# Kernel tuning notes

Measured on AMD Instinct MI355X. Metric: run time of the kernel, lower is better.

Reference implementation:

```python
import jax, jax.numpy as jnp
import numpy as np

LN_EPS = 1e-5
EPSILON = 1e-8
NUM_ITERS = 3
SLOT_SIZE = 128
NUM_SLOTS = 7
MLP_HIDDEN = 256


def _layernorm(x, g, b):
    m = jnp.mean(x, axis=-1, keepdims=True)
    v = jnp.var(x, axis=-1, keepdims=True)
    return (x - m) * jax.lax.rsqrt(v + LN_EPS) * g + b


def setup_inputs() -> dict:
    key = jax.random.key(0)
    ks = jax.random.split(key, 16)
    B, N, D, S, H, M = 64, 4096, 128, NUM_SLOTS, SLOT_SIZE, MLP_HIDDEN
    sc = 0.05
    return {
        "inputs": jax.random.normal(ks[0], (B, N, D), jnp.float32),
        "slots_init": jax.random.normal(ks[1], (B, S, H + 4), jnp.float32),
        "ln_in_g": jnp.ones((D,), jnp.float32), "ln_in_b": jnp.zeros((D,), jnp.float32),
        "ln_s_g": jnp.ones((H,), jnp.float32), "ln_s_b": jnp.zeros((H,), jnp.float32),
        "ln_m_g": jnp.ones((H,), jnp.float32), "ln_m_b": jnp.zeros((H,), jnp.float32),
        "Wq": jax.random.normal(ks[2], (H, H), jnp.float32) * sc,
        "Wk": jax.random.normal(ks[3], (H, H), jnp.float32) * sc,
        "Wv": jax.random.normal(ks[4], (H, H), jnp.float32) * sc,
        "W_ih": jax.random.normal(ks[5], (3 * H, H), jnp.float32) * sc,
        "W_hh": jax.random.normal(ks[6], (3 * H, H), jnp.float32) * sc,
        "b_ih": jnp.zeros((3 * H,), jnp.float32),
        "b_hh": jnp.zeros((3 * H,), jnp.float32),
        "mlp_w1": jax.random.normal(ks[7], (M, H), jnp.float32) * sc,
        "mlp_b1": jnp.zeros((M,), jnp.float32),
        "mlp_w2": jax.random.normal(ks[8], (H, M), jnp.float32) * sc,
        "mlp_b2": jnp.zeros((H,), jnp.float32),
        "slots_mu": jax.random.normal(ks[9], (1, 1, H + 4), jnp.float32) * sc,
        "slots_log_sigma": jax.random.normal(ks[10], (1, 1, H + 4), jnp.float32) * sc,
    }


def _gru_cell(x, h, W_ih, W_hh, b_ih, b_hh):
    # torch.nn.GRUCell math; x, h: [..., H]
    gi = x @ W_ih.T + b_ih
    gh = h @ W_hh.T + b_hh
    i_r, i_z, i_n = jnp.split(gi, 3, axis=-1)
    h_r, h_z, h_n = jnp.split(gh, 3, axis=-1)
    r = jax.nn.sigmoid(i_r + h_r)
    z = jax.nn.sigmoid(i_z + h_z)
    n = jnp.tanh(i_n + r * h_n)
    return (1.0 - z) * n + z * h


def reference(inputs, slots_init, ln_in_g, ln_in_b, ln_s_g, ln_s_b, ln_m_g, ln_m_b,
              Wq, Wk, Wv, W_ih, W_hh, b_ih, b_hh, mlp_w1, mlp_b1, mlp_w2, mlp_b2,
              slots_mu, slots_log_sigma):
    x = _layernorm(inputs, ln_in_g, ln_in_b)           # [B, N, D]
    k = x @ Wk.T                                       # [B, N, H]
    v = x @ Wv.T                                       # [B, N, H]
    slots_full = slots_mu + jnp.exp(slots_log_sigma) * slots_init  # [B, S, H+4]
    slots = slots_full[..., :SLOT_SIZE]                # positions/scales discarded
    scale = SLOT_SIZE ** -0.5
    for _ in range(NUM_ITERS):
        slots_prev = slots
        sn = _layernorm(slots, ln_s_g, ln_s_b)
        q = sn @ Wq.T                                  # [B, S, H]
        logits = scale * jnp.einsum('bnh,bsh->bns', k, q)
        attn = jax.nn.softmax(logits, axis=-1) + EPSILON
        attn = attn / jnp.sum(attn, axis=1, keepdims=True)
        updates = jnp.einsum('bns,bnh->bsh', attn, v)  # [B, S, H]
        slots = _gru_cell(updates, slots_prev, W_ih, W_hh, b_ih, b_hh)
        slots = slots + (jax.nn.relu(_layernorm(slots, ln_m_g, ln_m_b) @ mlp_w1.T + mlp_b1) @ mlp_w2.T + mlp_b2)
    return slots
```

## Files before the change

### kernel.cpp

```cpp
#include <hip/hip_runtime.h>
#include <hip/hip_bf16.h>
#include <stdint.h>

typedef unsigned int u32;
typedef unsigned short u16;
typedef float v2f __attribute__((ext_vector_type(2)));
typedef short bf16x8 __attribute__((ext_vector_type(8)));
typedef float f32x4 __attribute__((ext_vector_type(4)));

#define LN_EPS_ 1e-5f
#define EPS_ 1e-8f

__device__ __forceinline__ float bflo(u32 v){ return __uint_as_float(v << 16); }
__device__ __forceinline__ float bfhi(u32 v){ return __uint_as_float(v & 0xFFFF0000u); }
__device__ __forceinline__ u32 f2bf(float f){
    u32 x = __float_as_uint(f);
    return (x + 0x7FFFu + ((x >> 16) & 1u)) >> 16;
}
__device__ __forceinline__ u32 pack2bf(float a, float b){
    union { __hip_bfloat162 h; u32 u; } cv;
    cv.h = __float22bfloat162_rn(float2{a, b});
    return cv.u;
}
__device__ __forceinline__ v2f pkfma(v2f a, v2f b, v2f c){
    v2f d; asm("v_pk_fma_f32 %0, %1, %2, %3" : "=v"(d) : "v"(a), "v"(b), "v"(c)); return d;
}
__device__ __forceinline__ v2f pkadd(v2f a, v2f b){
    v2f d; asm("v_pk_add_f32 %0, %1, %2" : "=v"(d) : "v"(a), "v"(b)); return d;
}
__device__ __forceinline__ bf16x8 as_bf16x8(uint4 u){
    union { uint4 a; bf16x8 b; } c; c.a = u; return c.b;
}

__global__ __launch_bounds__(256) void k_pack(
    const float* __restrict__ Wq, const float* __restrict__ Wv,
    const float* __restrict__ Wih, const float* __restrict__ Whh,
    const float* __restrict__ w1, const float* __restrict__ w2,
    float* __restrict__ WqT, u32* __restrict__ Pv, u32* __restrict__ Pih,
    u32* __restrict__ Phh, u32* __restrict__ Pw1, u32* __restrict__ Pw2,
    u32* __restrict__ Rg32)
{
    int i = blockIdx.x * 256 + threadIdx.x;
    if (i < 8192) {
        int dp = i >> 7, o = i & 127;
        Pv[i] = pack2bf(Wv[o * 128 + 2 * dp], Wv[o * 128 + 2 * dp + 1]);
    } else if (i < 32768) {
        int r = i - 8192; int dp = r / 384, j = r - dp * 384;
        Pih[r] = pack2bf(Wih[j * 128 + 2 * dp], Wih[j * 128 + 2 * dp + 1]);
    } else if (i < 57344) {
        int r = i - 32768; int dp = r / 384, j = r - dp * 384;
        Phh[r] = pack2bf(Whh[j * 128 + 2 * dp], Whh[j * 128 + 2 * dp + 1]);
    } else if (i < 73728) {
        int r = i - 57344; int dp = r >> 8, j = r & 255;
        Pw1[r] = pack2bf(w1[j * 128 + 2 * dp], w1[j * 128 + 2 * dp + 1]);
    } else if (i < 90112) {
        int r = i - 73728; int mp = r >> 7, o = r & 127;
        Pw2[r] = pack2bf(w2[o * 256 + 2 * mp], w2[o * 256 + 2 * mp + 1]);
    } else if (i < 106496) {
        int r = i - 90112; int d = r >> 7, o = r & 127;
        WqT[r] = Wq[o * 128 + d];
    } else if (i < 143360) {
        int r = i - 106496; int b = r / 576, rem = r - b * 576;
        Rg32[b * 1024 + 448 + rem] = 0;
    }
}

__device__ __forceinline__ void prep_tail(
    int b, int s, int h, int half, int t, float nv,
    const float* __restrict__ g_s, const float* __restrict__ b_s,
    const float* __restrict__ WqT, const float* __restrict__ Wk,
    const float* __restrict__ g_in, const float* __restrict__ b_in,
    u16* __restrict__ Rg, float* __restrict__ c1ws, float* __restrict__ c2ws,
    float* snb, float* qb, float* xch, float* red4)
{
    if (!half) {
        float smv = nv, sqv = nv * nv;
        for (int m = 32; m >= 1; m >>= 1) { smv += __shfl_xor(smv, m); sqv += __shfl_xor(sqv, m); }
        if ((t & 63) == 0) { red4[(t >> 6) * 2] = smv; red4[(t >> 6) * 2 + 1] = sqv; }
    }
    __syncthreads();
    float mean = (red4[0] + red4[2]) * (1.0f / 128.0f);
    float var  = (red4[1] + red4[3]) * (1.0f / 128.0f) - mean * mean;
    float rsv = rsqrtf(var + LN_EPS_);
    if (!half) snb[h] = (nv - mean) * rsv * g_s[h] + b_s[h];
    __syncthreads();
    {
        float q0 = 0.f, q1 = 0.f;
        int d0 = half * 64;
        #pragma unroll 4
        for (int d = d0; d < d0 + 64; d += 2) {
            q0 += WqT[d * 128 + h] * snb[d];
            q1 += WqT[(d + 1) * 128 + h] * snb[d + 1];
        }
        if (half) xch[h] = q0 + q1;
        __syncthreads();
        if (!half) qb[h] = q0 + q1 + xch[h];
        __syncthreads();
    }
    float r0 = 0.f, r1 = 0.f;
    int j0 = half * 64;
    #pragma unroll 4
    for (int j = j0; j < j0 + 64; j += 2) {
        r0 += Wk[j * 128 + h] * qb[j];
        r1 += Wk[(j + 1) * 128 + h] * qb[j + 1];
    }
    if (half) xch[h] = r0 + r1;
    __syncthreads();
    if (!half) {
        float r = (r0 + r1 + xch[h]) * 0.08838834764831845f;
        float rt  = g_in[h] * r;
        float c2v = b_in[h] * r;
        Rg[((size_t)b * 16 + s) * 128 + h] = (u16)f2bf(rt);
        float c1p = rt, c2p = c2v;
        for (int m = 32; m >= 1; m >>= 1) { c1p += __shfl_xor(c1p, m); c2p += __shfl_xor(c2p, m); }
        if ((t & 63) == 0) { red4[(t >> 6) * 2] = c1p; red4[(t >> 6) * 2 + 1] = c2p; }
    }
    __syncthreads();
    if (t == 0) {
        c1ws[b * 8 + s] = red4[0] + red4[2];
        c2ws[b * 8 + s] = red4[1] + red4[3];
    }
}

__global__ __launch_bounds__(256) void k_init_prep(
    const float* __restrict__ slots_init, const float* __restrict__ mu,
    const float* __restrict__ ls, float* __restrict__ slots,
    const float* __restrict__ g_s, const float* __restrict__ b_s,
    const float* __restrict__ WqT, const float* __restrict__ Wk,
    const float* __restrict__ g_in, const float* __restrict__ b_in,
    u16* __restrict__ Rg, float* __restrict__ c1ws, float* __restrict__ c2ws)
{
    __shared__ float snb[128], qb[128], xch[128], red4[4];
    int bs = blockIdx.x, t = threadIdx.x;
    int b = bs / 7, s = bs - b * 7;
    int h = t & 127, half = t >> 7;
    float nv = 0.f;
    if (!half) {
        nv = mu[h] + expf(ls[h]) * slots_init[bs * 132 + h];
        slots[bs * 128 + h] = nv;
    }
    prep_tail(b, s, h, half, t, nv, g_s, b_s, WqT, Wk, g_in, b_in,
              Rg, c1ws, c2ws, snb, qb, xch, red4);
}

__global__ __launch_bounds__(256, 8) void k_attn(
    const float* __restrict__ xin,
    const u16* __restrict__ Rg, const float* __restrict__ c1ws,
    const float* __restrict__ c2ws,
    float* __restrict__ ypart, float* __restrict__ Zp, float* __restrict__ Ap)
{
    __shared__ u32 tile[4096];
    __shared__ __align__(16) float wt[448];
    __shared__ __align__(8)  float stats[128];
    __shared__ float c1l[16], c2l[16];
    __shared__ float redp[4][8], redw[4][8];
    int t = threadIdx.x;
    int b = blockIdx.y;
    int n0 = blockIdx.x * 64;
    int lane = t & 63, wv = t >> 6;
    int ls = lane & 15, lg = lane >> 4;

    if (t < 16) {
        c1l[t] = (t < 7) ? c1ws[b * 8 + t] : 0.f;
        c2l[t] = (t < 7) ? c2ws[b * 8 + t] : 0.f;
    }

    bf16x8 bfr[4];
    {
        const u16* Rrow = Rg + ((size_t)b * 16 + ls) * 128;
        #pragma unroll
        for (int kk = 0; kk < 4; kk++)
            bfr[kk] = as_bf16x8(*(const uint4*)&Rrow[kk * 32 + lg * 8]);
    }

    {
        int r = t >> 2, p = t & 3;
        const float4* xg = (const float4*)(xin + ((size_t)b * 4096 + n0 + r) * 128 + p * 32);
        v2f smp = (v2f){0.f, 0.f}, sqp = (v2f){0.f, 0.f};
        #pragma unroll
        for (int i = 0; i < 8; i++) {
            float4 v = xg[i];
            v2f lo = (v2f){v.x, v.y}, hi = (v2f){v.z, v.w};
            smp = pkadd(smp, pkadd(lo, hi));
            sqp = pkfma(lo, lo, sqp);
            sqp = pkfma(hi, hi, sqp);
            int q = p * 4 + (i >> 1), rem = (i & 1) * 2;
            *(uint2*)&tile[(r * 16 + (q ^ (r & 15))) * 4 + rem] =
                make_uint2(pack2bf(v.x, v.y), pack2bf(v.z, v.w));
        }
        float sm = smp.x + smp.y, sq = sqp.x + sqp.y;
        sm += __shfl_xor(sm, 1); sq += __shfl_xor(sq, 1);
        sm += __shfl_xor(sm, 2); sq += __shfl_xor(sq, 2);
        if (!p) {
            float mean = sm * (1.0f / 128.0f);
            float var  = sq * (1.0f / 128.0f) - mean * mean;
            *(float2*)&stats[2 * r] = make_float2(mean, rsqrtf(var + LN_EPS_));
        }
    }
    __syncthreads();

    f32x4 acc0 = {0.f, 0.f, 0.f, 0.f};
    {
        int m0 = wv * 16 + ls;
        #pragma unroll
        for (int kk = 0; kk < 4; kk++) {
            int q = kk * 4 + lg;
            bf16x8 a0 = as_bf16x8(*(const uint4*)&tile[(m0 * 16 + (q ^ ls)) * 4]);
            acc0 = __builtin_amdgcn_mfma_f32_16x16x32_bf16(a0, bfr[kk], acc0, 0, 0, 0);
        }
    }
    {
        float zsum = 0.f, asum = 0.f;
        float c1v = c1l[ls], c2v = c2l[ls];
        bool sv = ls < 7;
        int nbase = wv * 16 + lg * 4;
        #pragma unroll
        for (int r4 = 0; r4 < 4; r4++) {
            int n = nbase + r4;
            float2 stf = *(const float2*)&stats[2 * n];
            float L = sv ? (stf.y * (acc0[r4] - stf.x * c1v) + c2v) : -3.4e38f;
            float mx = L;
            mx = fmaxf(mx, __shfl_xor(mx, 1));
            mx = fmaxf(mx, __shfl_xor(mx, 2));
            mx = fmaxf(mx, __shfl_xor(mx, 4));
            mx = fmaxf(mx, __shfl_xor(mx, 8));
            float e = __expf(L - mx);
            float ssum = e;
            ssum += __shfl_xor(ssum, 1);
            ssum += __shfl_xor(ssum, 2);
            ssum += __shfl_xor(ssum, 4);
            ssum += __shfl_xor(ssum, 8);
            float p = e * (1.0f / ssum) + EPS_;
            float w = p * stf.y;
            if (sv) {
                wt[ls * 64 + n] = w;
                zsum += p;
                asum += w * stf.x;
            }
        }
        zsum += __shfl_xor(zsum, 16); zsum += __shfl_xor(zsum, 32);
        asum += __shfl_xor(asum, 16); asum += __shfl_xor(asum, 32);
        if (lane < 7) { redp[wv][lane] = zsum; redw[wv][lane] = asum; }
    }
    __syncthreads();
    if (t < 7)
        Zp[((size_t)b * 64 + blockIdx.x) * 8 + t] =
            redp[0][t] + redp[1][t] + redp[2][t] + redp[3][t];
    else if (t >= 64 && t < 71) {
        int s = t - 64;
        Ap[((size_t)b * 64 + blockIdx.x) * 8 + s] =
            redw[0][s] + redw[1][s] + redw[2][s] + redw[3][s];
    }

    int nh = t >> 7, dp = t & 63, sA = (t >> 6) & 1;
    v2f aclo[4], achi[4];
    #pragma unroll
    for (int k = 0; k < 4; k++) { aclo[k] = (v2f){0.f,0.f}; achi[k] = (v2f){0.f,0.f}; }
    int nbeg = nh * 32;
    #pragma unroll 4
    for (int n = nbeg; n < nbeg + 32; n += 2) {
        u32 x0 = tile[(n * 16 + ((dp >> 2) ^ (n & 15))) * 4 + (dp & 3)];
        u32 x1 = tile[((n + 1) * 16 + ((dp >> 2) ^ ((n + 1) & 15))) * 4 + (dp & 3)];
        v2f alo = (v2f){bflo(x0), bflo(x1)};
        v2f ahi = (v2f){bfhi(x0), bfhi(x1)};
        #pragma unroll
        for (int k = 0; k < 4; k++) {
            int s = sA + 2 * k;
            if (s < 7) {
                v2f wp = *(const v2f*)&wt[s * 64 + n];
                aclo[k] = pkfma(alo, wp, aclo[k]);
                achi[k] = pkfma(ahi, wp, achi[k]);
            }
        }
    }
    float* yp = ypart + (((size_t)b * 64 + blockIdx.x) * 2 + nh) * 896;
    #pragma unroll
    for (int k = 0; k < 4; k++) {
        int s = sA + 2 * k;
        if (s < 7) {
            *(float2*)&yp[s * 128 + 2 * dp] =
                make_float2(aclo[k].x + aclo[k].y, achi[k].x + achi[k].y);
        }
    }
}

__global__ __launch_bounds__(256) void k_update(
    float* __restrict__ slots, const float* __restrict__ ypart,
    const float* __restrict__ Zp, const float* __restrict__ Ap,
    const float* __restrict__ g_in, const float* __restrict__ b_in,
    const u32* __restrict__ Pv, const u32* __restrict__ Pih,
    const u32* __restrict__ Phh, const float* __restrict__ b_ih,
    const float* __restrict__ b_hh, const float* __restrict__ g_m,
    const float* __restrict__ b_m, const u32* __restrict__ Pw1,
    const float* __restrict__ bb1, const u32* __restrict__ Pw2,
    const float* __restrict__ bb2, float* __restrict__ out,
    const float* __restrict__ g_s, const float* __restrict__ b_s,
    const float* __restrict__ WqT, const float* __restrict__ Wk,
    u16* __restrict__ Rg, float* __restrict__ c1ws, float* __restrict__ c2ws,
    int do_prep)
{
    __shared__ float ybuf[128], ub[128], hb[128], lb[128], t1b[256];
    __shared__ float ghx[384];
    __shared__ float up[128], op[128];
    __shared__ float redA[2], redB[2];
    __shared__ float snb[128], qb[128], xch[128], red4[4];
    __shared__ float Zsh, Ash;
    int bs = blockIdx.x, t = threadIdx.x;
    int b = bs / 7, s = bs - b * 7;
    int h = t & 127, half = t >> 7;
    float ysum = 0.f;
    {
        const float* bp = ypart + ((size_t)(b * 128 + half * 64)) * 896 + s * 128 + h;
        #pragma unroll 8
        for (int c = 0; c < 64; c++) ysum += bp[(size_t)c * 896];
    }
    if (t < 64) {
        float z = Zp[((size_t)b * 64 + t) * 8 + s];
        for (int m = 32; m >= 1; m >>= 1) z += __shfl_xor(z, m);
        if (t == 0) Zsh = z;
    } else if (t < 128) {
        float a_ = Ap[((size_t)b * 64 + (t - 64)) * 8 + s];
        for (int m = 32; m >= 1; m >>= 1) a_ += __shfl_xor(a_, m);
        if (t == 64) Ash = a_;
    }
    if (half) up[h] = ysum;
    __syncthreads();
    if (!half) {
        float ytot = ysum + up[h];
        ybuf[h] = g_in[h] * (ytot - Ash) / Zsh + b_in[h];
        hb[h] = slots[bs * 128 + h];
    }
    __syncthreads();
    {
        float a0 = 0.f, a1 = 0.f;
        int dp0 = half * 32;
        #pragma unroll 4
        for (int dp = dp0; dp < dp0 + 32; dp += 2) {
            u32 w0 = Pv[dp * 128 + h];
            u32 w1v = Pv[(dp + 1) * 128 + h];
            a0 += bflo(w0) * ybuf[2 * dp] + bfhi(w0) * ybuf[2 * dp + 1];
            a1 += bflo(w1v) * ybuf[2 * dp + 2] + bfhi(w1v) * ybuf[2 * dp + 3];
        }
        if (half) up[h] = a0 + a1;
        __syncthreads();
        if (!half) ub[h] = (a0 + a1) + up[h];
        __syncthreads();
    }
    float gv0, gv1, gv2;
    {
        const u32* P = half ? Phh : Pih;
        const float* src = half ? hb : ub;
        gv0 = half ? b_hh[h] : b_ih[h];
        gv1 = half ? b_hh[128 + h] : b_ih[128 + h];
        gv2 = half ? b_hh[256 + h] : b_ih[256 + h];
        #pragma unroll 4
        for (int dp = 0; dp < 64; dp++) {
            float x0 = src[2 * dp], x1 = src[2 * dp + 1];
            u32 w0 = P[dp * 384 + h];
            u32 w1v = P[dp * 384 + 128 + h];
            u32 w2v = P[dp * 384 + 256 + h];
            gv0 += bflo(w0) * x0 + bfhi(w0) * x1;
            gv1 += bflo(w1v) * x0 + bfhi(w1v) * x1;
            gv2 += bflo(w2v) * x0 + bfhi(w2v) * x1;
        }
        if (half) { ghx[h] = gv0; ghx[128 + h] = gv1; ghx[256 + h] = gv2; }
    }
    __syncthreads();
    float hv = 0.f;
    if (!half) {
        float rg = 1.0f / (1.0f + __expf(-(gv0 + ghx[h])));
        float zg = 1.0f / (1.0f + __expf(-(gv1 + ghx[128 + h])));
        float ng = tanhf(gv2 + rg * ghx[256 + h]);
        hv = (1.0f - zg) * ng + zg * hb[h];
        float sm2 = hv, sq2 = hv * hv;
        for (int m = 32; m >= 1; m >>= 1) { sm2 += __shfl_xor(sm2, m); sq2 += __shfl_xor(sq2, m); }
        if ((t & 63) == 0) { redA[t >> 6] = sm2; redB[t >> 6] = sq2; }
    }
    __syncthreads();
    if (!half) {
        float sm2 = redA[0] + redA[1], sq2 = redB[0] + redB[1];
        float mean = sm2 * (1.0f / 128.0f);
        float var  = sq2 * (1.0f / 128.0f) - mean * mean;
        float rsq = rsqrtf(var + LN_EPS_);
        lb[h] = (hv - mean) * rsq * g_m[h] + b_m[h];
    }
    __syncthreads();
    {
        float m1 = bb1[t];
        #pragma unroll 4
        for (int dp = 0; dp < 64; dp++) {
            u32 w0 = Pw1[dp * 256 + t];
            m1 += bflo(w0) * lb[2 * dp] + bfhi(w0) * lb[2 * dp + 1];
        }
        t1b[t] = fmaxf(m1, 0.0f);
    }
    __syncthreads();
    float nv = 0.f;
    {
        float o0 = 0.f, o1 = 0.f;
        int mp0 = half * 64;
        #pragma unroll 4
        for (int mp = mp0; mp < mp0 + 64; mp += 2) {
            u32 w0 = Pw2[mp * 128 + h];
            u32 w1v = Pw2[(mp + 1) * 128 + h];
            o0 += bflo(w0) * t1b[2 * mp] + bfhi(w0) * t1b[2 * mp + 1];
            o1 += bflo(w1v) * t1b[2 * mp + 2] + bfhi(w1v) * t1b[2 * mp + 3];
        }
        if (half) op[h] = o0 + o1;
        __syncthreads();
        if (!half) {
            nv = hv + bb2[h] + (o0 + o1) + op[h];
            slots[bs * 128 + h] = nv;
            out[bs * 128 + h] = nv;
        }
    }
    if (do_prep) {
        __syncthreads();
        prep_tail(b, s, h, half, t, nv, g_s, b_s, WqT, Wk, g_in, b_in,
                  Rg, c1ws, c2ws, snb, qb, xch, red4);
    }
}

extern "C" void kernel_launch(void* const* d_in, const int* in_sizes, int n_in,
                              void* d_out, int out_size, void* d_ws, size_t ws_size,
                              hipStream_t stream) {
    const float* inputs     = (const float*)d_in[0];
    const float* slots_init = (const float*)d_in[1];
    const float* ln_in_g    = (const float*)d_in[2];
    const float* ln_in_b    = (const float*)d_in[3];
    const float* ln_s_g     = (const float*)d_in[4];
    const float* ln_s_b     = (const float*)d_in[5];
    const float* ln_m_g     = (const float*)d_in[6];
    const float* ln_m_b     = (const float*)d_in[7];
    const float* Wq         = (const float*)d_in[8];
    const float* Wk         = (const float*)d_in[9];
    const float* Wv         = (const float*)d_in[10];
    const float* W_ih       = (const float*)d_in[11];
    const float* W_hh       = (const float*)d_in[12];
    const float* b_ih       = (const float*)d_in[13];
    const float* b_hh       = (const float*)d_in[14];
    const float* mlp_w1     = (const float*)d_in[15];
    const float* mlp_b1     = (const float*)d_in[16];
    const float* mlp_w2     = (const float*)d_in[17];
    const float* mlp_b2     = (const float*)d_in[18];
    const float* slots_mu   = (const float*)d_in[19];
    const float* slots_ls   = (const float*)d_in[20];

    char* ws = (char*)d_ws;
    float* slots = (float*)(ws);
    u16*   Rg    = (u16*)  (ws + 229376);
    float* c1ws  = (float*)(ws + 491520);
    float* c2ws  = (float*)(ws + 493568);
    float* WqT   = (float*)(ws + 495616);
    u32*   Pv    = (u32*)  (ws + 561152);
    u32*   Pih   = (u32*)  (ws + 593920);
    u32*   Phh   = (u32*)  (ws + 692224);
    u32*   Pw1   = (u32*)  (ws + 790528);
    u32*   Pw2   = (u32*)  (ws + 856064);
    float* Zp    = (float*)(ws + 921600);
    float* Ap    = (float*)(ws + 1052672);
    float* ypart = (float*)(ws + 1183744);

    k_pack<<<560, 256, 0, stream>>>(Wq, Wv, W_ih, W_hh, mlp_w1, mlp_w2,
                                    WqT, Pv, Pih, Phh, Pw1, Pw2, (u32*)Rg);
    k_init_prep<<<448, 256, 0, stream>>>(slots_init, slots_mu, slots_ls, slots,
                                         ln_s_g, ln_s_b, WqT, Wk, ln_in_g, ln_in_b,
                                         Rg, c1ws, c2ws);
    for (int it = 0; it < 3; it++) {
        k_attn<<<dim3(64, 64), 256, 0, stream>>>(inputs, Rg, c1ws, c2ws,
                                                 ypart, Zp, Ap);
        k_update<<<448, 256, 0, stream>>>(slots, ypart, Zp, Ap, ln_in_g, ln_in_b,
                                          Pv, Pih, Phh, b_ih, b_hh,
                                          ln_m_g, ln_m_b, Pw1, mlp_b1, Pw2, mlp_b2,
                                          (float*)d_out,
                                          ln_s_g, ln_s_b, WqT, Wk,
                                          Rg, c1ws, c2ws, (it < 2) ? 1 : 0);
    }
}
```

Before: 388.4 us.

## Cache bf16 swizzled input tiles and LN stats after first attention pass

On the first attention iteration, each block writes its already-swizzled bf16 tile and per-row layernorm stats to a workspace buffer. Later iterations reload these instead of re-reading the fp32 inputs and recomputing statistics, halving input bytes per pass. The update kernel also moves from 256 to 512 threads, splitting each matvec four ways with shared-memory reductions. The trade-off is extra workspace traffic on the first pass, and it assumes the workspace is large enough at the new offsets.

```diff
diff --git a/kernel.cpp b/kernel.cpp
--- a/kernel.cpp
+++ b/kernel.cpp
@@ -65,63 +65,6 @@
     }
 }
 
-__device__ __forceinline__ void prep_tail(
-    int b, int s, int h, int half, int t, float nv,
-    const float* __restrict__ g_s, const float* __restrict__ b_s,
-    const float* __restrict__ WqT, const float* __restrict__ Wk,
-    const float* __restrict__ g_in, const float* __restrict__ b_in,
-    u16* __restrict__ Rg, float* __restrict__ c1ws, float* __restrict__ c2ws,
-    float* snb, float* qb, float* xch, float* red4)
-{
-    if (!half) {
-        float smv = nv, sqv = nv * nv;
-        for (int m = 32; m >= 1; m >>= 1) { smv += __shfl_xor(smv, m); sqv += __shfl_xor(sqv, m); }
-        if ((t & 63) == 0) { red4[(t >> 6) * 2] = smv; red4[(t >> 6) * 2 + 1] = sqv; }
-    }
-    __syncthreads();
-    float mean = (red4[0] + red4[2]) * (1.0f / 128.0f);
-    float var  = (red4[1] + red4[3]) * (1.0f / 128.0f) - mean * mean;
-    float rsv = rsqrtf(var + LN_EPS_);
-    if (!half) snb[h] = (nv - mean) * rsv * g_s[h] + b_s[h];
-    __syncthreads();
-    {
-        float q0 = 0.f, q1 = 0.f;
-        int d0 = half * 64;
-        #pragma unroll 4
-        for (int d = d0; d < d0 + 64; d += 2) {
-            q0 += WqT[d * 128 + h] * snb[d];
-            q1 += WqT[(d + 1) * 128 + h] * snb[d + 1];
-        }
-        if (half) xch[h] = q0 + q1;
-        __syncthreads();
-        if (!half) qb[h] = q0 + q1 + xch[h];
-        __syncthreads();
-    }
-    float r0 = 0.f, r1 = 0.f;
-    int j0 = half * 64;
-    #pragma unroll 4
-    for (int j = j0; j < j0 + 64; j += 2) {
-        r0 += Wk[j * 128 + h] * qb[j];
-        r1 += Wk[(j + 1) * 128 + h] * qb[j + 1];
-    }
-    if (half) xch[h] = r0 + r1;
-    __syncthreads();
-    if (!half) {
-        float r = (r0 + r1 + xch[h]) * 0.08838834764831845f;
-        float rt  = g_in[h] * r;
-        float c2v = b_in[h] * r;
-        Rg[((size_t)b * 16 + s) * 128 + h] = (u16)f2bf(rt);
-        float c1p = rt, c2p = c2v;
-        for (int m = 32; m >= 1; m >>= 1) { c1p += __shfl_xor(c1p, m); c2p += __shfl_xor(c2p, m); }
-        if ((t & 63) == 0) { red4[(t >> 6) * 2] = c1p; red4[(t >> 6) * 2 + 1] = c2p; }
-    }
-    __syncthreads();
-    if (t == 0) {
-        c1ws[b * 8 + s] = red4[0] + red4[2];
-        c2ws[b * 8 + s] = red4[1] + red4[3];
-    }
-}
-
 __global__ __launch_bounds__(256) void k_init_prep(
     const float* __restrict__ slots_init, const float* __restrict__ mu,
     const float* __restrict__ ls, float* __restrict__ slots,
@@ -139,15 +82,61 @@
         nv = mu[h] + expf(ls[h]) * slots_init[bs * 132 + h];
         slots[bs * 128 + h] = nv;
     }
-    prep_tail(b, s, h, half, t, nv, g_s, b_s, WqT, Wk, g_in, b_in,
-              Rg, c1ws, c2ws, snb, qb, xch, red4);
+    if (!half) {
+        float smv = nv, sqv = nv * nv;
+        for (int m = 32; m >= 1; m >>= 1) { smv += __shfl_xor(smv, m); sqv += __shfl_xor(sqv, m); }
+        if ((t & 63) == 0) { red4[(t >> 6) * 2] = smv; red4[(t >> 6) * 2 + 1] = sqv; }
+    }
+    __syncthreads();
+    float mean = (red4[0] + red4[2]) * (1.0f / 128.0f);
+    float var  = (red4[1] + red4[3]) * (1.0f / 128.0f) - mean * mean;
+    float rsv = rsqrtf(var + LN_EPS_);
+    if (!half) snb[h] = (nv - mean) * rsv * g_s[h] + b_s[h];
+    __syncthreads();
+    {
+        float q0 = 0.f, q1 = 0.f;
+        int d0 = half * 64;
+        #pragma unroll 4
+        for (int d = d0; d < d0 + 64; d += 2) {
+            q0 += WqT[d * 128 + h] * snb[d];
+            q1 += WqT[(d + 1) * 128 + h] * snb[d + 1];
+        }
+        if (half) xch[h] = q0 + q1;
+        __syncthreads();
+        if (!half) qb[h] = q0 + q1 + xch[h];
+        __syncthreads();
+    }
+    float r0 = 0.f, r1 = 0.f;
+    int j0 = half * 64;
+    #pragma unroll 4
+    for (int j = j0; j < j0 + 64; j += 2) {
+        r0 += Wk[j * 128 + h] * qb[j];
+        r1 += Wk[(j + 1) * 128 + h] * qb[j + 1];
+    }
+    if (half) xch[h] = r0 + r1;
+    __syncthreads();
+    if (!half) {
+        float r = (r0 + r1 + xch[h]) * 0.08838834764831845f;
+        float rt  = g_in[h] * r;
+        float c2v = b_in[h] * r;
+        Rg[((size_t)b * 16 + s) * 128 + h] = (u16)f2bf(rt);
+        float c1p = rt, c2p = c2v;
+        for (int m = 32; m >= 1; m >>= 1) { c1p += __shfl_xor(c1p, m); c2p += __shfl_xor(c2p, m); }
+        if ((t & 63) == 0) { red4[(t >> 6) * 2] = c1p; red4[(t >> 6) * 2 + 1] = c2p; }
+    }
+    __syncthreads();
+    if (t == 0) {
+        c1ws[b * 8 + s] = red4[0] + red4[2];
+        c2ws[b * 8 + s] = red4[1] + red4[3];
+    }
 }
 
 __global__ __launch_bounds__(256, 8) void k_attn(
     const float* __restrict__ xin,
     const u16* __restrict__ Rg, const float* __restrict__ c1ws,
     const float* __restrict__ c2ws,
-    float* __restrict__ ypart, float* __restrict__ Zp, float* __restrict__ Ap)
+    float* __restrict__ ypart, float* __restrict__ Zp, float* __restrict__ Ap,
+    u32* __restrict__ Xbf, float* __restrict__ Sg, int first)
 {
     __shared__ u32 tile[4096];
     __shared__ __align__(16) float wt[448];
@@ -159,6 +148,7 @@
     int n0 = blockIdx.x * 64;
     int lane = t & 63, wv = t >> 6;
     int ls = lane & 15, lg = lane >> 4;
+    size_t blk = (size_t)b * 64 + blockIdx.x;
 
     if (t < 16) {
         c1l[t] = (t < 7) ? c1ws[b * 8 + t] : 0.f;
@@ -173,7 +163,7 @@
             bfr[kk] = as_bf16x8(*(const uint4*)&Rrow[kk * 32 + lg * 8]);
     }
 
-    {
+    if (first) {
         int r = t >> 2, p = t & 3;
         const float4* xg = (const float4*)(xin + ((size_t)b * 4096 + n0 + r) * 128 + p * 32);
         v2f smp = (v2f){0.f, 0.f}, sqp = (v2f){0.f, 0.f};
@@ -196,8 +186,20 @@
             float var  = sq * (1.0f / 128.0f) - mean * mean;
             *(float2*)&stats[2 * r] = make_float2(mean, rsqrtf(var + LN_EPS_));
         }
-    }
-    __syncthreads();
+        __syncthreads();
+        uint4* dst = (uint4*)(Xbf + blk * 4096);
+        const uint4* srcT = (const uint4*)tile;
+        #pragma unroll
+        for (int j = 0; j < 4; j++) dst[j * 256 + t] = srcT[j * 256 + t];
+        if (t < 128) Sg[blk * 128 + t] = stats[t];
+    } else {
+        uint4* dstT = (uint4*)tile;
+        const uint4* src = (const uint4*)(Xbf + blk * 4096);
+        #pragma unroll
+        for (int j = 0; j < 4; j++) dstT[j * 256 + t] = src[j * 256 + t];
+        if (t < 128) stats[t] = Sg[blk * 128 + t];
+        __syncthreads();
+    }
 
     f32x4 acc0 = {0.f, 0.f, 0.f, 0.f};
     {
@@ -244,12 +246,10 @@
     }
     __syncthreads();
     if (t < 7)
-        Zp[((size_t)b * 64 + blockIdx.x) * 8 + t] =
-            redp[0][t] + redp[1][t] + redp[2][t] + redp[3][t];
+        Zp[blk * 8 + t] = redp[0][t] + redp[1][t] + redp[2][t] + redp[3][t];
     else if (t >= 64 && t < 71) {
         int s = t - 64;
-        Ap[((size_t)b * 64 + blockIdx.x) * 8 + s] =
-            redw[0][s] + redw[1][s] + redw[2][s] + redw[3][s];
+        Ap[blk * 8 + s] = redw[0][s] + redw[1][s] + redw[2][s] + redw[3][s];
     }
 
     int nh = t >> 7, dp = t & 63, sA = (t >> 6) & 1;
@@ -273,7 +273,7 @@
             }
         }
     }
-    float* yp = ypart + (((size_t)b * 64 + blockIdx.x) * 2 + nh) * 896;
+    float* yp = ypart + (blk * 2 + nh) * 896;
     #pragma unroll
     for (int k = 0; k < 4; k++) {
         int s = sA + 2 * k;
@@ -284,7 +284,7 @@
     }
 }
 
-__global__ __launch_bounds__(256) void k_update(
+__global__ __launch_bounds__(512) void k_update(
     float* __restrict__ slots, const float* __restrict__ ypart,
     const float* __restrict__ Zp, const float* __restrict__ Ap,
     const float* __restrict__ g_in, const float* __restrict__ b_in,
@@ -300,19 +300,21 @@
     int do_prep)
 {
     __shared__ float ybuf[128], ub[128], hb[128], lb[128], t1b[256];
-    __shared__ float ghx[384];
-    __shared__ float up[128], op[128];
+    __shared__ float red4w[4][128];
+    __shared__ float g6[12][128];
+    __shared__ float m1p[256];
     __shared__ float redA[2], redB[2];
-    __shared__ float snb[128], qb[128], xch[128], red4[4];
+    __shared__ float snb[128], qb[128], red4[4];
     __shared__ float Zsh, Ash;
     int bs = blockIdx.x, t = threadIdx.x;
     int b = bs / 7, s = bs - b * 7;
-    int h = t & 127, half = t >> 7;
-    float ysum = 0.f;
-    {
-        const float* bp = ypart + ((size_t)(b * 128 + half * 64)) * 896 + s * 128 + h;
+    int h = t & 127, q = t >> 7;
+    {
+        float ysum = 0.f;
+        const float* bp = ypart + ((size_t)(b * 128 + q * 32)) * 896 + s * 128 + h;
         #pragma unroll 8
-        for (int c = 0; c < 64; c++) ysum += bp[(size_t)c * 896];
+        for (int c = 0; c < 32; c++) ysum += bp[(size_t)c * 896];
+        red4w[q][h] = ysum;
     }
     if (t < 64) {
         float z = Zp[((size_t)b * 64 + t) * 8 + s];
@@ -323,38 +325,33 @@
         for (int m = 32; m >= 1; m >>= 1) a_ += __shfl_xor(a_, m);
         if (t == 64) Ash = a_;
     }
-    if (half) up[h] = ysum;
-    __syncthreads();
-    if (!half) {
-        float ytot = ysum + up[h];
+    __syncthreads();
+    if (q == 0) {
+        float ytot = red4w[0][h] + red4w[1][h] + red4w[2][h] + red4w[3][h];
         ybuf[h] = g_in[h] * (ytot - Ash) / Zsh + b_in[h];
         hb[h] = slots[bs * 128 + h];
     }
     __syncthreads();
     {
-        float a0 = 0.f, a1 = 0.f;
-        int dp0 = half * 32;
+        float a0 = 0.f;
+        int dp0 = q * 16;
         #pragma unroll 4
-        for (int dp = dp0; dp < dp0 + 32; dp += 2) {
+        for (int dp = dp0; dp < dp0 + 16; dp++) {
             u32 w0 = Pv[dp * 128 + h];
-            u32 w1v = Pv[(dp + 1) * 128 + h];
             a0 += bflo(w0) * ybuf[2 * dp] + bfhi(w0) * ybuf[2 * dp + 1];
-            a1 += bflo(w1v) * ybuf[2 * dp + 2] + bfhi(w1v) * ybuf[2 * dp + 3];
-        }
-        if (half) up[h] = a0 + a1;
-        __syncthreads();
-        if (!half) ub[h] = (a0 + a1) + up[h];
-        __syncthreads();
-    }
-    float gv0, gv1, gv2;
-    {
-        const u32* P = half ? Phh : Pih;
-        const float* src = half ? hb : ub;
-        gv0 = half ? b_hh[h] : b_ih[h];
-        gv1 = half ? b_hh[128 + h] : b_ih[128 + h];
-        gv2 = half ? b_hh[256 + h] : b_ih[256 + h];
+        }
+        red4w[q][h] = a0;
+    }
+    __syncthreads();
+    if (q == 0) ub[h] = red4w[0][h] + red4w[1][h] + red4w[2][h] + red4w[3][h];
+    __syncthreads();
+    {
+        const u32* P = (q >= 2) ? Phh : Pih;
+        const float* src = (q >= 2) ? hb : ub;
+        int dp0 = (q & 1) * 32;
+        float gv0 = 0.f, gv1 = 0.f, gv2 = 0.f;
         #pragma unroll 4
-        for (int dp = 0; dp < 64; dp++) {
+        for (int dp = dp0; dp < dp0 + 32; dp++) {
             float x0 = src[2 * dp], x1 = src[2 * dp + 1];
             u32 w0 = P[dp * 384 + h];
             u32 w1v = P[dp * 384 + 128 + h];
@@ -363,21 +360,27 @@
             gv1 += bflo(w1v) * x0 + bfhi(w1v) * x1;
             gv2 += bflo(w2v) * x0 + bfhi(w2v) * x1;
         }
-        if (half) { ghx[h] = gv0; ghx[128 + h] = gv1; ghx[256 + h] = gv2; }
+        g6[q * 3 + 0][h] = gv0; g6[q * 3 + 1][h] = gv1; g6[q * 3 + 2][h] = gv2;
     }
     __syncthreads();
     float hv = 0.f;
-    if (!half) {
-        float rg = 1.0f / (1.0f + __expf(-(gv0 + ghx[h])));
-        float zg = 1.0f / (1.0f + __expf(-(gv1 + ghx[128 + h])));
-        float ng = tanhf(gv2 + rg * ghx[256 + h]);
+    if (q == 0) {
+        float gi0 = g6[0][h] + g6[3][h] + b_ih[h];
+        float gi1 = g6[1][h] + g6[4][h] + b_ih[128 + h];
+        float gi2 = g6[2][h] + g6[5][h] + b_ih[256 + h];
+        float gh0 = g6[6][h] + g6[9][h]  + b_hh[h];
+        float gh1 = g6[7][h] + g6[10][h] + b_hh[128 + h];
+        float gh2 = g6[8][h] + g6[11][h] + b_hh[256 + h];
+        float rg = 1.0f / (1.0f + __expf(-(gi0 + gh0)));
+        float zg = 1.0f / (1.0f + __expf(-(gi1 + gh1)));
+        float ng = tanhf(gi2 + rg * gh2);
         hv = (1.0f - zg) * ng + zg * hb[h];
         float sm2 = hv, sq2 = hv * hv;
         for (int m = 32; m >= 1; m >>= 1) { sm2 += __shfl_xor(sm2, m); sq2 += __shfl_xor(sq2, m); }
         if ((t & 63) == 0) { redA[t >> 6] = sm2; redB[t >> 6] = sq2; }
     }
     __syncthreads();
-    if (!half) {
+    if (q == 0) {
         float sm2 = redA[0] + redA[1], sq2 = redB[0] + redB[1];
         float mean = sm2 * (1.0f / 128.0f);
         float var  = sq2 * (1.0f / 128.0f) - mean * mean;
@@ -386,38 +389,82 @@
     }
     __syncthreads();
     {
-        float m1 = bb1[t];
+        int o = t & 255, kh = t >> 8;
+        float m1 = 0.f;
+        int dp0 = kh * 32;
         #pragma unroll 4
-        for (int dp = 0; dp < 64; dp++) {
-            u32 w0 = Pw1[dp * 256 + t];
+        for (int dp = dp0; dp < dp0 + 32; dp++) {
+            u32 w0 = Pw1[dp * 256 + o];
             m1 += bflo(w0) * lb[2 * dp] + bfhi(w0) * lb[2 * dp + 1];
         }
-        t1b[t] = fmaxf(m1, 0.0f);
+        if (kh) m1p[o] = m1;
+        __syncthreads();
+        if (!kh) t1b[o] = fmaxf(m1 + m1p[o] + bb1[o], 0.0f);
+    }
+    __syncthreads();
+    {
+        float o0 = 0.f;
+        int mp0 = q * 32;
+        #pragma unroll 4
+        for (int mp = mp0; mp < mp0 + 32; mp++) {
+            u32 w0 = Pw2[mp * 128 + h];
+            o0 += bflo(w0) * t1b[2 * mp] + bfhi(w0) * t1b[2 * mp + 1];
+        }
+        red4w[q][h] = o0;
     }
     __syncthreads();
     float nv = 0.f;
-    {
-        float o0 = 0.f, o1 = 0.f;
-        int mp0 = half * 64;
-        #pragma unroll 4
-        for (int mp = mp0; mp < mp0 + 64; mp += 2) {
-            u32 w0 = Pw2[mp * 128 + h];
-            u32 w1v = Pw2[(mp + 1) * 128 + h];
-            o0 += bflo(w0) * t1b[2 * mp] + bfhi(w0) * t1b[2 * mp + 1];
-            o1 += bflo(w1v) * t1b[2 * mp + 2] + bfhi(w1v) * t1b[2 * mp + 3];
-        }
-        if (half) op[h] = o0 + o1;
-        __syncthreads();
-        if (!half) {
-            nv = hv + bb2[h] + (o0 + o1) + op[h];
-            slots[bs * 128 + h] = nv;
-            out[bs * 128 + h] = nv;
-        }
+    if (q == 0) {
+        nv = hv + bb2[h] + red4w[0][h] + red4w[1][h] + red4w[2][h] + red4w[3][h];
+        slots[bs * 128 + h] = nv;
+        out[bs * 128 + h] = nv;
     }
     if (do_prep) {
         __syncthreads();
-        prep_tail(b, s, h, half, t, nv, g_s, b_s, WqT, Wk, g_in, b_in,
-                  Rg, c1ws, c2ws, snb, qb, xch, red4);
+        if (q == 0) {
+            float smv = nv, sqv = nv * nv;
+            for (int m = 32; m >= 1; m >>= 1) { smv += __shfl_xor(smv, m); sqv += __shfl_xor(sqv, m); }
+            if ((t & 63) == 0) { red4[(t >> 6) * 2] = smv; red4[(t >> 6) * 2 + 1] = sqv; }
+        }
+        __syncthreads();
+        float mean = (red4[0] + red4[2]) * (1.0f / 128.0f);
+        float var  = (red4[1] + red4[3]) * (1.0f / 128.0f) - mean * mean;
+        float rsv = rsqrtf(var + LN_EPS_);
+        if (q == 0) snb[h] = (nv - mean) * rsv * g_s[h] + b_s[h];
+        __syncthreads();
+        {
+            float qv = 0.f;
+            int d0 = q * 32;
+            #pragma unroll 4
+            for (int d = d0; d < d0 + 32; d++) qv += WqT[d * 128 + h] * snb[d];
+            red4w[q][h] = qv;
+        }
+        __syncthreads();
+        if (q == 0) qb[h] = red4w[0][h] + red4w[1][h] + red4w[2][h] + red4w[3][h];
+        __syncthreads();
+        {
+            float rv = 0.f;
+            int j0 = q * 32;
+            #pragma unroll 4
+            for (int j = j0; j < j0 + 32; j++) rv += Wk[j * 128 + h] * qb[j];
+            red4w[q][h] = rv;
+        }
+        __syncthreads();
+        if (q == 0) {
+            float r = (red4w[0][h] + red4w[1][h] + red4w[2][h] + red4w[3][h])
+                      * 0.08838834764831845f;
+            float rt  = g_in[h] * r;
+            float c2v = b_in[h] * r;
+            Rg[((size_t)b * 16 + s) * 128 + h] = (u16)f2bf(rt);
+            float c1p = rt, c2p = c2v;
+            for (int m = 32; m >= 1; m >>= 1) { c1p += __shfl_xor(c1p, m); c2p += __shfl_xor(c2p, m); }
+            if ((t & 63) == 0) { red4[(t >> 6) * 2] = c1p; red4[(t >> 6) * 2 + 1] = c2p; }
+        }
+        __syncthreads();
+        if (t == 0) {
+            c1ws[b * 8 + s] = red4[0] + red4[2];
+            c2ws[b * 8 + s] = red4[1] + red4[3];
+        }
     }
 }
 
@@ -460,6 +507,8 @@
     float* Zp    = (float*)(ws + 921600);
     float* Ap    = (float*)(ws + 1052672);
     float* ypart = (float*)(ws + 1183744);
+    u32*   Xbf   = (u32*)  (ws + 30543872);
+    float* Sg    = (float*)(ws + 97652736);
 
     k_pack<<<560, 256, 0, stream>>>(Wq, Wv, W_ih, W_hh, mlp_w1, mlp_w2,
                                     WqT, Pv, Pih, Phh, Pw1, Pw2, (u32*)Rg);
@@ -468,8 +517,9 @@
                                          Rg, c1ws, c2ws);
     for (int it = 0; it < 3; it++) {
         k_attn<<<dim3(64, 64), 256, 0, stream>>>(inputs, Rg, c1ws, c2ws,
-                                                 ypart, Zp, Ap);
-        k_update<<<448, 256, 0, stream>>>(slots, ypart, Zp, Ap, ln_in_g, ln_in_b,
+                                                 ypart, Zp, Ap,
+                                                 Xbf, Sg, (it == 0) ? 1 : 0);
+        k_update<<<448, 512, 0, stream>>>(slots, ypart, Zp, Ap, ln_in_g, ln_in_b,
                                           Pv, Pih, Phh, b_ih, b_hh,
                                           ln_m_g, ln_m_b, Pw1, mlp_b1, Pw2, mlp_b2,
                                           (float*)d_out,
```

Result: slower. 402.6 us (+3.7%).
